# Performance work log

Hardware: AMD Instinct MI355X
Metric: run time of the kernel (lower is better)

Reference implementation:

```python
import jax, jax.numpy as jnp
import numpy as np

B, CIN, COUT, K, H, W = 16, 256, 256, 3, 64, 64
COND = 512


def setup_inputs() -> dict:
    key = jax.random.key(0)
    ks = jax.random.split(key, 10)
    X = jax.random.normal(ks[0], (B, CIN, H, W), dtype=jnp.float32)
    cond_v = jax.random.normal(ks[1], (B, COND), dtype=jnp.float32)
    # conv weight [O, I, kh, kw]
    conv_w = jax.random.normal(ks[2], (COUT, CIN, K, K), dtype=jnp.float32) / np.sqrt(CIN * K * K)
    w0 = jax.random.normal(ks[3], (COND, COND), dtype=jnp.float32) / np.sqrt(COND)
    b0 = jnp.zeros((COND,), dtype=jnp.float32)
    w1 = jax.random.normal(ks[4], (COND, COND), dtype=jnp.float32) / np.sqrt(COND)
    b1 = jnp.zeros((COND,), dtype=jnp.float32)
    w_out = jax.random.normal(ks[5], (CIN, COND), dtype=jnp.float32) / np.sqrt(COND)
    b_out = jnp.zeros((CIN,), dtype=jnp.float32)
    return {"X": X, "cond_v": cond_v, "conv_w": conv_w,
            "w0": w0, "b0": b0, "w1": w1, "b1": b1,
            "w_out": w_out, "b_out": b_out}


def reference(X, cond_v, conv_w, w0, b0, w1, b1, w_out, b_out):
    # proj_cond MLP: (Linear+SiLU) x depth, final Linear -> in_channels
    h = jax.nn.silu(cond_v @ w0.T + b0)
    h = jax.nn.silu(h @ w1.T + b1)
    scale = h @ w_out.T + b_out + 1.0          # [B, I]
    # modulate: bw[b,o,i,kh,kw] = w[o,i,kh,kw] * scale[b,i]
    bw = conv_w[None] * scale[:, None, :, None, None]
    # demodulate across (i, kh, kw)
    demod = jax.lax.rsqrt(jnp.sum(bw * bw, axis=(2, 3, 4)) + 1e-8)  # [B, O]
    bw = bw * demod[:, :, None, None, None]
    b, o, i, kh, kw = bw.shape
    # per-sample conv via grouped conv: x -> [1, B*I, H, W], w -> [B*O, I, kh, kw]
    x = X.reshape(1, b * i, X.shape[2], X.shape[3])
    w = bw.reshape(b * o, i, kh, kw)
    out = jax.lax.conv_general_dilated(
        x, w, window_strides=(1, 1), padding="SAME",
        feature_group_count=b,
        dimension_numbers=("NCHW", "OIHW", "NCHW"))
    return out.reshape(b, o, out.shape[2], out.shape[3])
```

## Files before the change

kernel.cpp:

```cpp
#include <hip/hip_runtime.h>
#include <hip/hip_bf16.h>
#include <cstdint>

#define NB 16
#define CI 256
#define CO 256
#define HH 64
#define WW 64
#define CC 512
#define HP 66
#define WP 66

typedef short short8 __attribute__((ext_vector_type(8)));
typedef float floatx4 __attribute__((ext_vector_type(4)));
typedef unsigned int uintx4 __attribute__((ext_vector_type(4)));

__device__ __forceinline__ void g2lds16(const void* g, void* l) {
  __builtin_amdgcn_global_load_lds((const __attribute__((address_space(1))) void*)g,
                                   (__attribute__((address_space(3))) void*)l, 16, 0, 0);
}

#define ASM_VMCNT0() do { __builtin_amdgcn_sched_barrier(0);            \
                          asm volatile("s_waitcnt vmcnt(0)" ::: "memory"); \
                          __builtin_amdgcn_sched_barrier(0); } while (0)
#define RAW_BAR() do { __builtin_amdgcn_sched_barrier(0);  \
                       __builtin_amdgcn_s_barrier();       \
                       __builtin_amdgcn_sched_barrier(0); } while (0)

template<int KD, int N, bool SILU, bool PLUSONE, int BJ>
__global__ void k_mlp(const float* __restrict__ in, const float* __restrict__ w,
                      const float* __restrict__ bias, float* __restrict__ out) {
  __shared__ float4 sin4[KD / 4];
  const int nb = N / BJ;
  int b = blockIdx.x / nb;
  int j = (blockIdx.x % nb) * BJ + threadIdx.x;
  const float4* in4 = reinterpret_cast<const float4*>(in + (size_t)b * KD);
  for (int k = threadIdx.x; k < KD / 4; k += BJ) sin4[k] = in4[k];
  __syncthreads();
  float acc = bias[j];
  const float4* wr = reinterpret_cast<const float4*>(w + (size_t)j * KD);
#pragma unroll 8
  for (int kk = 0; kk < KD / 4; ++kk) {
    float4 wv = wr[kk];
    float4 sv = sin4[kk];
    acc += wv.x * sv.x + wv.y * sv.y + wv.z * sv.z + wv.w * sv.w;
  }
  if (SILU) acc = acc / (1.0f + __expf(-acc));
  if (PLUSONE) acc += 1.0f;
  out[(size_t)b * N + j] = acc;
}

__global__ void k_repack(const float* __restrict__ cw, __hip_bfloat16* __restrict__ Wt,
                         float* __restrict__ wsq) {
  int gid = blockIdx.x * 256 + threadIdx.x;
  if (gid >= CO * CI) return;
  const float* p = cw + (size_t)gid * 9;
  float s = 0.0f;
#pragma unroll
  for (int t = 0; t < 9; ++t) {
    float v = p[t];
    s += v * v;
    Wt[(size_t)t * CO * CI + gid] = __float2bfloat16(v);
  }
  wsq[gid] = s;
}

__global__ void k_demod(const float* __restrict__ wsq, const float* __restrict__ scale,
                        float* __restrict__ demod) {
  __shared__ float s2[CI];
  int b = blockIdx.x;
  int o = threadIdx.x;
  float sv = scale[b * CI + o];
  s2[o] = sv * sv;
  __syncthreads();
  float acc = 0.0f;
  const float4* wr = reinterpret_cast<const float4*>(wsq + (size_t)o * CI);
  const float4* s4 = reinterpret_cast<const float4*>(s2);
#pragma unroll 8
  for (int i = 0; i < CI / 4; ++i) {
    float4 wv = wr[i];
    float4 sq = s4[i];
    acc += wv.x * sq.x + wv.y * sq.y + wv.z * sq.z + wv.w * sq.w;
  }
  demod[b * CO + o] = rsqrtf(acc + 1e-8f);
}

__global__ void k_scalex(const float* __restrict__ X, const float* __restrict__ scale,
                         __hip_bfloat16* __restrict__ Xs) {
  __shared__ float tile[64][68];
  __shared__ float ssc[64];
  int bid = blockIdx.x;
  int b = bid >> 8;
  int rem = bid & 255;
  int h = rem >> 2;
  int i0 = (rem & 3) * 64;
  int t = threadIdx.x;
  if (t < 64) ssc[t] = scale[b * CI + i0 + t];

  __hip_bfloat16* xs_img = Xs + (size_t)b * HP * WP * CI;
  uintx4 z = {0u, 0u, 0u, 0u};
  if (t < 16) {
    int px = (t >> 3) * 65;
    int sl = t & 7;
    *reinterpret_cast<uintx4*>(xs_img + (((size_t)(h + 1)) * WP + px) * CI + i0 + sl * 8) = z;
  }
  if (h == 0) {
    for (int u = t; u < 66 * 8; u += 256) {
      int px = u >> 3, sl = u & 7;
      *reinterpret_cast<uintx4*>(xs_img + ((size_t)px) * CI + i0 + sl * 8) = z;
    }
  }
  if (h == 63) {
    for (int u = t; u < 66 * 8; u += 256) {
      int px = u >> 3, sl = u & 7;
      *reinterpret_cast<uintx4*>(xs_img + ((size_t)65 * WP + px) * CI + i0 + sl * 8) = z;
    }
  }

  const float* src = X + (((size_t)b * CI + i0) * HH + h) * WW;
  int ii_base = t >> 4;
  int w4 = (t & 15) * 4;
#pragma unroll
  for (int r2 = 0; r2 < 4; ++r2) {
    int ii = r2 * 16 + ii_base;
    int key = ((ii >> 3) & 7) << 2;
    *reinterpret_cast<float4*>(&tile[ii][w4 ^ key]) =
        *reinterpret_cast<const float4*>(src + (size_t)ii * HH * WW + w4);
  }
  __syncthreads();
  int u = t & 7;
  int wl = t >> 3;
  int key = u << 2;
#pragma unroll
  for (int iter = 0; iter < 2; ++iter) {
    int w2 = wl + iter * 32;
    union { unsigned short us[8]; uintx4 v; } pk;
#pragma unroll
    for (int j = 0; j < 8; ++j) {
      int ii = u * 8 + j;
      float v = tile[ii][w2 ^ key] * ssc[ii];
      __hip_bfloat16 hb = __float2bfloat16(v);
      pk.us[j] = *reinterpret_cast<unsigned short*>(&hb);
    }
    *reinterpret_cast<uintx4*>(xs_img + (((size_t)(h + 1)) * WP + (w2 + 1)) * CI + i0 + u * 8) = pk.v;
  }
}

__global__ __launch_bounds__(256, 1)
void k_conv(const __hip_bfloat16* __restrict__ Xs, const __hip_bfloat16* __restrict__ Wt,
            const float* __restrict__ demod, float* __restrict__ out) {
  __shared__ __align__(16) char lds[2 * 28672];
  char* sX0 = lds;

  int wg = (blockIdx.x & 7) * 64 + (blockIdx.x >> 3);
  int b = wg >> 5;
  int rem = wg & 31;
  int ht = rem >> 1;
  int ob = rem & 1;
  int h0 = ht * 4;
  int o0 = ob * 128;

  int tid = threadIdx.x;
  int wv = tid >> 6;
  int lane = tid & 63;
  int lhi = lane >> 4;
  int llo = lane & 15;
  int wo2 = wv >> 1;
  int wpx = wv & 1;

  floatx4 acc[4][8];
#pragma unroll
  for (int m = 0; m < 4; ++m)
#pragma unroll
    for (int n = 0; n < 8; ++n) acc[m][n] = (floatx4){0.f, 0.f, 0.f, 0.f};

  const __hip_bfloat16* xs_img = Xs + (size_t)b * HP * WP * CI;

  int xoff[7];
#pragma unroll
  for (int s = 0; s < 7; ++s) {
    int j = wv + 4 * s;
    int pr = 16 * j + (lane >> 2);
    int prc = pr > 431 ? 431 : pr;
    int lr = prc / 72;
    int wp = prc - lr * 72;
    if (wp > 65) wp = 65;
    int ksl = (lane & 3) ^ ((pr >> 1) & 3);
    xoff[s] = ((h0 + lr) * WP + wp) * CI + ksl * 8;
  }
  int aofs[4];
#pragma unroll
  for (int m = 0; m < 4; ++m)
    aofs[m] = (o0 + wo2 * 64 + m * 16 + llo) * CI + lhi * 8;

  short8 bqA[8], bqB[8];
  short8 afA[4], afB[4];

#define TAP(c, t, CUR, NXT) do {                                                          \
    if ((t) <= 6 && (c) < 7)                                                              \
      g2lds16(xs_img + xoff[(t)] + ((c) + 1) * 32,                                        \
              sX0 + (((c) + 1) & 1) * 28672 + (wv + 4 * (t)) * 1024);                     \
    if (!((c) == 7 && (t) == 8)) {                                                        \
      const __hip_bfloat16* wb_ = Wt +                                                    \
          (size_t)(((t) == 8) ? 0 : (t) + 1) * CO * CI +                                  \
          (size_t)(((t) == 8) ? (c) + 1 : (c)) * 32;                                      \
      af##NXT[0] = *reinterpret_cast<const short8*>(wb_ + aofs[0]);                       \
      af##NXT[1] = *reinterpret_cast<const short8*>(wb_ + aofs[1]);                       \
      af##NXT[2] = *reinterpret_cast<const short8*>(wb_ + aofs[2]);                       \
      af##NXT[3] = *reinterpret_cast<const short8*>(wb_ + aofs[3]);                       \
    }                                                                                     \
    if ((t) < 8) {                                                                        \
      const char* xb_ = sX0 + ((c) & 1) * 28672;                                          \
      const int kh_ = ((t) + 1) / 3, kw_ = ((t) + 1) % 3;                                 \
      _Pragma("unroll")                                                                   \
      for (int n = 0; n < 8; ++n) {                                                       \
        int prl = (wpx * 2 + (n >> 2) + kh_) * 72 + (n & 3) * 16 + llo + kw_;             \
        bq##NXT[n] = *reinterpret_cast<const short8*>(                                    \
            xb_ + prl * 64 + ((lhi ^ ((prl >> 1) & 3)) << 4));                            \
      }                                                                                   \
    }                                                                                     \
    __builtin_amdgcn_s_setprio(1);                                                        \
    _Pragma("unroll")                                                                     \
    for (int n = 0; n < 8; ++n) {                                                         \
      _Pragma("unroll")                                                                   \
      for (int m = 0; m < 4; ++m)                                                         \
        acc[m][n] = __builtin_amdgcn_mfma_f32_16x16x32_bf16(af##CUR[m], bq##CUR[n],       \
                                                            acc[m][n], 0, 0, 0);          \
    }                                                                                     \
    __builtin_amdgcn_s_setprio(0);                                                        \
  } while (0)

#define CHUNK_END(c, NXT) do {                                                            \
    if ((c) < 7) {                                                                        \
      ASM_VMCNT0();                                                                       \
      RAW_BAR();                                                                          \
      const char* xb_ = sX0 + (((c) + 1) & 1) * 28672;                                    \
      _Pragma("unroll")                                                                   \
      for (int n = 0; n < 8; ++n) {                                                       \
        int prl = (wpx * 2 + (n >> 2)) * 72 + (n & 3) * 16 + llo;                         \
        bq##NXT[n] = *reinterpret_cast<const short8*>(                                    \
            xb_ + prl * 64 + ((lhi ^ ((prl >> 1) & 3)) << 4));                            \
      }                                                                                   \
    }                                                                                     \
  } while (0)

#define CHUNK_EVEN(c) do {                                                                \
    TAP(c,0,A,B); TAP(c,1,B,A); TAP(c,2,A,B); TAP(c,3,B,A); TAP(c,4,A,B);                 \
    TAP(c,5,B,A); TAP(c,6,A,B); TAP(c,7,B,A); TAP(c,8,A,B);                               \
    CHUNK_END(c, B); } while (0)
#define CHUNK_ODD(c) do {                                                                 \
    TAP(c,0,B,A); TAP(c,1,A,B); TAP(c,2,B,A); TAP(c,3,A,B); TAP(c,4,B,A);                 \
    TAP(c,5,A,B); TAP(c,6,B,A); TAP(c,7,A,B); TAP(c,8,B,A);                               \
    CHUNK_END(c, A); } while (0)

#pragma unroll
  for (int s = 0; s < 7; ++s)
    g2lds16(xs_img + xoff[s], sX0 + (wv + 4 * s) * 1024);
#pragma unroll
  for (int m = 0; m < 4; ++m)
    afA[m] = *reinterpret_cast<const short8*>(Wt + aofs[m]);
  ASM_VMCNT0();
  RAW_BAR();
#pragma unroll
  for (int n = 0; n < 8; ++n) {
    int prl = (wpx * 2 + (n >> 2)) * 72 + (n & 3) * 16 + llo;
    bqA[n] = *reinterpret_cast<const short8*>(
        sX0 + prl * 64 + ((lhi ^ ((prl >> 1) & 3)) << 4));
  }

  for (int c2 = 0; c2 < 8; c2 += 2) {
    CHUNK_EVEN(c2);
    CHUNK_ODD(c2 + 1);
  }

#pragma unroll
  for (int m = 0; m < 4; ++m) {
    int obase_o = o0 + wo2 * 64 + m * 16 + lhi * 4;
    float4 dmv = *reinterpret_cast<const float4*>(demod + (size_t)b * CO + obase_o);
#pragma unroll
    for (int j = 0; j < 4; ++j) {
      int o = obase_o + j;
      float dm = (j == 0) ? dmv.x : (j == 1) ? dmv.y : (j == 2) ? dmv.z : dmv.w;
      float* orow = out + (((size_t)b * CO + o) * HH + h0) * WW;
#pragma unroll
      for (int n = 0; n < 8; ++n) {
        int row = wpx * 2 + (n >> 2);
        int col = (n & 3) * 16 + llo;
        orow[(size_t)row * WW + col] = acc[m][n][j] * dm;
      }
    }
  }
#undef TAP
#undef CHUNK_END
#undef CHUNK_EVEN
#undef CHUNK_ODD
}

extern "C" void kernel_launch(void* const* d_in, const int* in_sizes, int n_in,
                              void* d_out, int out_size, void* d_ws, size_t ws_size,
                              hipStream_t stream) {
  const float* X      = (const float*)d_in[0];
  const float* cond_v = (const float*)d_in[1];
  const float* conv_w = (const float*)d_in[2];
  const float* w0     = (const float*)d_in[3];
  const float* b0     = (const float*)d_in[4];
  const float* w1     = (const float*)d_in[5];
  const float* b1     = (const float*)d_in[6];
  const float* w_out  = (const float*)d_in[7];
  const float* b_out  = (const float*)d_in[8];
  float* out = (float*)d_out;

  char* ws = (char*)d_ws;
  const size_t XS_BYTES  = (size_t)NB * HP * WP * CI * 2;
  const size_t WT_BYTES  = (size_t)9 * CO * CI * 2;
  const size_t WSQ_BYTES = (size_t)CO * CI * 4;
  __hip_bfloat16* Xs = (__hip_bfloat16*)ws;
  __hip_bfloat16* Wt = (__hip_bfloat16*)(ws + XS_BYTES);
  float* wsq   = (float*)(ws + XS_BYTES + WT_BYTES);
  float* h0b   = (float*)(ws + XS_BYTES + WT_BYTES + WSQ_BYTES);
  float* h1b   = h0b + NB * CC;
  float* scale = h1b + NB * CC;
  float* demod = scale + NB * CI;

  k_repack<<<(CO * CI) / 256, 256, 0, stream>>>(conv_w, Wt, wsq);
  k_mlp<CC, CC, true, false, 128><<<NB * (CC / 128), 128, 0, stream>>>(cond_v, w0, b0, h0b);
  k_mlp<CC, CC, true, false, 128><<<NB * (CC / 128), 128, 0, stream>>>(h0b, w1, b1, h1b);
  k_mlp<CC, CI, false, true, 128><<<NB * (CI / 128), 128, 0, stream>>>(h1b, w_out, b_out, scale);
  k_demod<<<NB, CO, 0, stream>>>(wsq, scale, demod);
  k_scalex<<<NB * 64 * 4, 256, 0, stream>>>(X, scale, Xs);
  k_conv<<<NB * 32, 256, 0, stream>>>(Xs, Wt, demod, out);
}
```

Before: 161.2 us.

## Remap conv warps to full output-channel tiles and allow two blocks per CU

Each wave now computes all 128 output channels for one output row (8x4 MFMA tiles) instead of 64 channels by two rows, so the weight fragments loaded from global are shared across more pixels and the B operand is loaded fresh per tap from LDS without double buffering. Launch bounds are raised to two workgroups per CU to improve latency hiding, and the chunk-end wait is relaxed from vmcnt(0) to vmcnt(8) so outstanding weight loads need not drain before the barrier. The change trades more per-wave A-fragment registers and global weight loads for fewer LDS reads, and it risks register pressure or spilling under the tighter occupancy bound. The relaxed wait relies on the LDS copies being issued before the eight weight loads.

```diff
diff --git a/kernel.cpp b/kernel.cpp
--- a/kernel.cpp
+++ b/kernel.cpp
@@ -22,6 +22,9 @@
 
 #define ASM_VMCNT0() do { __builtin_amdgcn_sched_barrier(0);            \
                           asm volatile("s_waitcnt vmcnt(0)" ::: "memory"); \
+                          __builtin_amdgcn_sched_barrier(0); } while (0)
+#define ASM_VMCNT8() do { __builtin_amdgcn_sched_barrier(0);            \
+                          asm volatile("s_waitcnt vmcnt(8)" ::: "memory"); \
                           __builtin_amdgcn_sched_barrier(0); } while (0)
 #define RAW_BAR() do { __builtin_amdgcn_sched_barrier(0);  \
                        __builtin_amdgcn_s_barrier();       \
@@ -146,7 +149,7 @@
   }
 }
 
-__global__ __launch_bounds__(256, 1)
+__global__ __launch_bounds__(256, 2)
 void k_conv(const __hip_bfloat16* __restrict__ Xs, const __hip_bfloat16* __restrict__ Wt,
             const float* __restrict__ demod, float* __restrict__ out) {
   __shared__ __align__(16) char lds[2 * 28672];
@@ -165,14 +168,12 @@
   int lane = tid & 63;
   int lhi = lane >> 4;
   int llo = lane & 15;
-  int wo2 = wv >> 1;
-  int wpx = wv & 1;
-
-  floatx4 acc[4][8];
-#pragma unroll
-  for (int m = 0; m < 4; ++m)
-#pragma unroll
-    for (int n = 0; n < 8; ++n) acc[m][n] = (floatx4){0.f, 0.f, 0.f, 0.f};
+
+  floatx4 acc[8][4];
+#pragma unroll
+  for (int m = 0; m < 8; ++m)
+#pragma unroll
+    for (int n = 0; n < 4; ++n) acc[m][n] = (floatx4){0.f, 0.f, 0.f, 0.f};
 
   const __hip_bfloat16* xs_img = Xs + (size_t)b * HP * WP * CI;
 
@@ -188,13 +189,13 @@
     int ksl = (lane & 3) ^ ((pr >> 1) & 3);
     xoff[s] = ((h0 + lr) * WP + wp) * CI + ksl * 8;
   }
-  int aofs[4];
-#pragma unroll
-  for (int m = 0; m < 4; ++m)
-    aofs[m] = (o0 + wo2 * 64 + m * 16 + llo) * CI + lhi * 8;
-
-  short8 bqA[8], bqB[8];
-  short8 afA[4], afB[4];
+  int aofs[8];
+#pragma unroll
+  for (int m = 0; m < 8; ++m)
+    aofs[m] = (o0 + m * 16 + llo) * CI + lhi * 8;
+
+  short8 afA[8], afB[8];
+  short8 bq[4];
 
 #define TAP(c, t, CUR, NXT) do {                                                          \
     if ((t) <= 6 && (c) < 7)                                                              \
@@ -204,69 +205,52 @@
       const __hip_bfloat16* wb_ = Wt +                                                    \
           (size_t)(((t) == 8) ? 0 : (t) + 1) * CO * CI +                                  \
           (size_t)(((t) == 8) ? (c) + 1 : (c)) * 32;                                      \
-      af##NXT[0] = *reinterpret_cast<const short8*>(wb_ + aofs[0]);                       \
-      af##NXT[1] = *reinterpret_cast<const short8*>(wb_ + aofs[1]);                       \
-      af##NXT[2] = *reinterpret_cast<const short8*>(wb_ + aofs[2]);                       \
-      af##NXT[3] = *reinterpret_cast<const short8*>(wb_ + aofs[3]);                       \
+      _Pragma("unroll")                                                                   \
+      for (int m = 0; m < 8; ++m)                                                         \
+        af##NXT[m] = *reinterpret_cast<const short8*>(wb_ + aofs[m]);                     \
     }                                                                                     \
-    if ((t) < 8) {                                                                        \
+    {                                                                                     \
       const char* xb_ = sX0 + ((c) & 1) * 28672;                                          \
-      const int kh_ = ((t) + 1) / 3, kw_ = ((t) + 1) % 3;                                 \
+      const int kh_ = (t) / 3, kw_ = (t) % 3;                                             \
       _Pragma("unroll")                                                                   \
-      for (int n = 0; n < 8; ++n) {                                                       \
-        int prl = (wpx * 2 + (n >> 2) + kh_) * 72 + (n & 3) * 16 + llo + kw_;             \
-        bq##NXT[n] = *reinterpret_cast<const short8*>(                                    \
+      for (int n = 0; n < 4; ++n) {                                                       \
+        int prl = (wv + kh_) * 72 + n * 16 + llo + kw_;                                   \
+        bq[n] = *reinterpret_cast<const short8*>(                                         \
             xb_ + prl * 64 + ((lhi ^ ((prl >> 1) & 3)) << 4));                            \
       }                                                                                   \
     }                                                                                     \
     __builtin_amdgcn_s_setprio(1);                                                        \
     _Pragma("unroll")                                                                     \
-    for (int n = 0; n < 8; ++n) {                                                         \
+    for (int n = 0; n < 4; ++n) {                                                         \
       _Pragma("unroll")                                                                   \
-      for (int m = 0; m < 4; ++m)                                                         \
-        acc[m][n] = __builtin_amdgcn_mfma_f32_16x16x32_bf16(af##CUR[m], bq##CUR[n],       \
+      for (int m = 0; m < 8; ++m)                                                         \
+        acc[m][n] = __builtin_amdgcn_mfma_f32_16x16x32_bf16(af##CUR[m], bq[n],            \
                                                             acc[m][n], 0, 0, 0);          \
     }                                                                                     \
     __builtin_amdgcn_s_setprio(0);                                                        \
   } while (0)
 
-#define CHUNK_END(c, NXT) do {                                                            \
-    if ((c) < 7) {                                                                        \
-      ASM_VMCNT0();                                                                       \
-      RAW_BAR();                                                                          \
-      const char* xb_ = sX0 + (((c) + 1) & 1) * 28672;                                    \
-      _Pragma("unroll")                                                                   \
-      for (int n = 0; n < 8; ++n) {                                                       \
-        int prl = (wpx * 2 + (n >> 2)) * 72 + (n & 3) * 16 + llo;                         \
-        bq##NXT[n] = *reinterpret_cast<const short8*>(                                    \
-            xb_ + prl * 64 + ((lhi ^ ((prl >> 1) & 3)) << 4));                            \
-      }                                                                                   \
-    }                                                                                     \
+#define CHUNK_END(c) do {                                                                 \
+    if ((c) < 7) { ASM_VMCNT8(); RAW_BAR(); }                                             \
   } while (0)
 
 #define CHUNK_EVEN(c) do {                                                                \
     TAP(c,0,A,B); TAP(c,1,B,A); TAP(c,2,A,B); TAP(c,3,B,A); TAP(c,4,A,B);                 \
     TAP(c,5,B,A); TAP(c,6,A,B); TAP(c,7,B,A); TAP(c,8,A,B);                               \
-    CHUNK_END(c, B); } while (0)
+    CHUNK_END(c); } while (0)
 #define CHUNK_ODD(c) do {                                                                 \
     TAP(c,0,B,A); TAP(c,1,A,B); TAP(c,2,B,A); TAP(c,3,A,B); TAP(c,4,B,A);                 \
     TAP(c,5,A,B); TAP(c,6,B,A); TAP(c,7,A,B); TAP(c,8,B,A);                               \
-    CHUNK_END(c, A); } while (0)
+    CHUNK_END(c); } while (0)
 
 #pragma unroll
   for (int s = 0; s < 7; ++s)
     g2lds16(xs_img + xoff[s], sX0 + (wv + 4 * s) * 1024);
 #pragma unroll
-  for (int m = 0; m < 4; ++m)
+  for (int m = 0; m < 8; ++m)
     afA[m] = *reinterpret_cast<const short8*>(Wt + aofs[m]);
-  ASM_VMCNT0();
+  ASM_VMCNT8();
   RAW_BAR();
-#pragma unroll
-  for (int n = 0; n < 8; ++n) {
-    int prl = (wpx * 2 + (n >> 2)) * 72 + (n & 3) * 16 + llo;
-    bqA[n] = *reinterpret_cast<const short8*>(
-        sX0 + prl * 64 + ((lhi ^ ((prl >> 1) & 3)) << 4));
-  }
 
   for (int c2 = 0; c2 < 8; c2 += 2) {
     CHUNK_EVEN(c2);
@@ -274,20 +258,16 @@
   }
 
 #pragma unroll
-  for (int m = 0; m < 4; ++m) {
-    int obase_o = o0 + wo2 * 64 + m * 16 + lhi * 4;
-    float4 dmv = *reinterpret_cast<const float4*>(demod + (size_t)b * CO + obase_o);
+  for (int m = 0; m < 8; ++m) {
+    int ob_o = o0 + m * 16 + lhi * 4;
+    float4 dmv = *reinterpret_cast<const float4*>(demod + (size_t)b * CO + ob_o);
 #pragma unroll
     for (int j = 0; j < 4; ++j) {
-      int o = obase_o + j;
       float dm = (j == 0) ? dmv.x : (j == 1) ? dmv.y : (j == 2) ? dmv.z : dmv.w;
-      float* orow = out + (((size_t)b * CO + o) * HH + h0) * WW;
-#pragma unroll
-      for (int n = 0; n < 8; ++n) {
-        int row = wpx * 2 + (n >> 2);
-        int col = (n & 3) * 16 + llo;
-        orow[(size_t)row * WW + col] = acc[m][n][j] * dm;
-      }
+      float* orow = out + (((size_t)b * CO + ob_o + j) * HH + (h0 + wv)) * WW;
+#pragma unroll
+      for (int n = 0; n < 4; ++n)
+        orow[n * 16 + llo] = acc[m][n][j] * dm;
     }
   }
 #undef TAP
```

New measurement: 251.3 us. 1.56x slower.
